# Performance work log

Measured on AMD Instinct MI355X. Metric: run time of the kernel, lower is better.

## Reference

```python
import jax, jax.numpy as jnp
import numpy as np

NUM_USERS = 100000
NUM_RATINGS = 5
EMBED_DIM = 64
ATT_DIM = 16
B, G, L, S = 16384, 8, 50, 32


def setup_inputs() -> dict:
    key = jax.random.key(0)
    ks = jax.random.split(key, 16)
    inp = {
        # forward args (int / bool constants)
        "nodes": jax.random.randint(ks[0], (B, G), 0, NUM_USERS),
        "history_u": jax.random.randint(ks[1], (B, L), 0, NUM_USERS),
        "history_r": jax.random.randint(ks[2], (B, L), 0, NUM_RATINGS),
        "history_mask": jax.random.randint(ks[3], (B, L), 0, 2).astype(bool).at[:, 0].set(True),
        "social_adj": jax.random.randint(ks[4], (B, S), 0, NUM_USERS),
        "social_mask": jax.random.randint(ks[5], (B, S), 0, 2).astype(bool).at[:, 0].set(True),
        # learned parameters
        "features": jax.random.normal(ks[6], (NUM_USERS, EMBED_DIM), jnp.float32) * 0.02,
        "r_embed": jax.random.normal(ks[7], (NUM_RATINGS, EMBED_DIM), jnp.float32) * 0.02,
        "wg1": jax.random.normal(ks[8], (EMBED_DIM, ATT_DIM), jnp.float32) / np.sqrt(EMBED_DIM),
        "bg1": jnp.zeros((ATT_DIM,), jnp.float32),
        "wg2": jax.random.normal(ks[9], (ATT_DIM, 1), jnp.float32) / np.sqrt(ATT_DIM),
        "bg2": jnp.zeros((1,), jnp.float32),
        "w1": jax.random.normal(ks[10], (2 * EMBED_DIM, EMBED_DIM), jnp.float32) / np.sqrt(2 * EMBED_DIM),
        "b1": jnp.zeros((EMBED_DIM,), jnp.float32),
    }
    return inp


def _masked_mean(x, mask):
    # x: [B, N, D], mask: [B, N] float -> [B, D]
    denom = jnp.maximum(mask.sum(axis=1, keepdims=True), 1.0)
    return (x * mask[..., None]).sum(axis=1) / denom


def reference(nodes, history_u, history_r, history_mask, social_adj, social_mask,
              features, r_embed, wg1, bg1, wg2, bg2, w1, b1):
    dt = features.dtype
    # --- Group_Embedding: attention pooling over member embeddings ---
    members = features[nodes]                              # [B, G, D] gather
    h = jnp.tanh(members @ wg1 + bg1)                      # [B, G, 16]
    logits = (h @ wg2 + bg2)[..., 0]                       # [B, G]
    alpha = jax.nn.softmax(logits, axis=-1)
    self_feats = jnp.einsum('bg,bgd->bd', alpha, members)  # [B, D]

    # --- aggregator: ragged history (item+rating) + social neighbor means ---
    hm = history_mask.astype(dt)
    hist = features[history_u] + r_embed[history_r]        # [B, L, D] gather
    hist_mean = _masked_mean(hist, hm)                     # [B, D]

    sm = social_mask.astype(dt)
    soc_mean = _masked_mean(features[social_adj], sm)      # [B, D]

    neigh_feats = 0.5 * (hist_mean + soc_mean)             # [B, D]

    # --- concat -> linear -> relu ---
    combined = jnp.concatenate([self_feats, neigh_feats], axis=1)  # [B, 2D]
    return jax.nn.relu(combined @ w1 + b1)                 # [B, D]
```

## Files before the change

kernel.cpp:

```cpp
#include <hip/hip_runtime.h>
#include <cstdint>
#include <cstddef>

#define NUSERS 100000
#define BB 16384

static __device__ __forceinline__ float readlane_f(float v, int l) {
    return __uint_as_float(__builtin_amdgcn_readlane(__float_as_uint(v), l));
}
static __device__ __forceinline__ int readlane_i(int v, int l) {
    return __builtin_amdgcn_readlane(v, l);
}

__global__ __launch_bounds__(256) void k0_scores(
    const float* __restrict__ features, const float* __restrict__ wg1,
    const float* __restrict__ bg1, const float* __restrict__ wg2,
    const float* __restrict__ bg2, float* __restrict__ Q)
{
    __shared__ float frow[16 * 68];
    __shared__ float wg1t[16 * 68];
    const int tid = threadIdx.x;
    const int blk = blockIdx.x;
    const float* fbase = features + (size_t)blk * 16 * 64;
    for (int i = tid; i < 1024; i += 256) {
        frow[(i >> 6) * 68 + (i & 63)] = fbase[i];
        wg1t[(i & 15) * 68 + (i >> 4)] = wg1[i];
    }
    __syncthreads();
    const int k = tid & 15, ul = tid >> 4;
    float x = bg1[k];
    #pragma unroll
    for (int d4 = 0; d4 < 16; ++d4) {
        const float4 f = *(const float4*)&frow[ul * 68 + d4 * 4];
        const float4 w = *(const float4*)&wg1t[k * 68 + d4 * 4];
        x += f.x * w.x + f.y * w.y + f.z * w.z + f.w * w.w;
    }
    float xx = fminf(fmaxf(x, -9.f), 9.f);
    float e2 = __expf(2.f * xx);
    float th = (e2 - 1.f) / (e2 + 1.f);
    float t = th * wg2[k];
    t += __shfl_xor(t, 1);
    t += __shfl_xor(t, 2);
    t += __shfl_xor(t, 4);
    t += __shfl_xor(t, 8);
    if (k == 0) Q[blk * 16 + ul] = t + bg2[0];
}

__global__ __launch_bounds__(256) void k1_fuse(
    const int* __restrict__ nodes, const int* __restrict__ hist_u,
    const int* __restrict__ hist_r, const int* __restrict__ hist_m,
    const int* __restrict__ soc_a, const int* __restrict__ soc_m,
    const float* __restrict__ features, const float* __restrict__ r_embed,
    const float* __restrict__ Q, float* __restrict__ comb)
{
    __shared__ int hcomp[4][64];
    __shared__ int scomp[4][32];

    const int tid = threadIdx.x;
    const int lane = tid & 63;
    const int wv = tid >> 6;
    const int e = blockIdx.x * 4 + wv;

    const float re0 = r_embed[0 * 64 + lane];
    const float re1 = r_embed[1 * 64 + lane];
    const float re2 = r_embed[2 * 64 + lane];
    const float re3 = r_embed[3 * 64 + lane];
    const float re4 = r_embed[4 * 64 + lane];

    int nd = (lane < 8) ? nodes[e * 8 + lane] : 0;
    int hu = 0, hr = 0, hmv = 0;
    if (lane < 50) {
        hu  = hist_u[e * 50 + lane];
        hr  = hist_r[e * 50 + lane];
        hmv = hist_m[e * 50 + lane];
    }
    int sa = 0, sk = 0;
    if (lane < 32) {
        sa = soc_a[e * 32 + lane];
        sk = soc_m[e * 32 + lane];
    }

    uint64_t hb = __ballot(hmv != 0);
    const int hc = (int)__popcll(hb);
    int hrank = (int)__popcll(hb & ((1ull << lane) - 1));
    if (hmv) hcomp[wv][hrank] = hu << 8;

    uint64_t sbm = __ballot(sk != 0);
    const int scn = (int)__popcll(sbm);
    int srank = (int)__popcll(sbm & ((1ull << lane) - 1));
    if (sk) scomp[wv][srank] = sa << 8;

    const int c0 = (int)__popcll(__ballot(hmv && hr == 0));
    const int c1 = (int)__popcll(__ballot(hmv && hr == 1));
    const int c2 = (int)__popcll(__ballot(hmv && hr == 2));
    const int c3 = (int)__popcll(__ballot(hmv && hr == 3));
    const int c4 = (int)__popcll(__ballot(hmv && hr == 4));

    float m[8];
    #pragma unroll
    for (int g = 0; g < 8; ++g) {
        int idx = readlane_i(nd, g);
        m[g] = features[idx * 64 + lane];
    }
    float sc = (lane < 8) ? Q[nd] : -1e30f;
    float mx = sc;
    mx = fmaxf(mx, __shfl_xor(mx, 1));
    mx = fmaxf(mx, __shfl_xor(mx, 2));
    mx = fmaxf(mx, __shfl_xor(mx, 4));
    float ex = __expf(sc - mx);
    float sm = ex;
    sm += __shfl_xor(sm, 1);
    sm += __shfl_xor(sm, 2);
    sm += __shfl_xor(sm, 4);
    float al = ex / sm;
    float sf = 0.f;
    #pragma unroll
    for (int g = 0; g < 8; ++g)
        sf += readlane_f(al, g) * m[g];

    int hpk = hcomp[wv][lane];
    int spk = scomp[wv][lane & 31];

    float a0 = 0.f, a1 = 0.f, a2 = 0.f, a3 = 0.f;
    int i = 0;
    for (; i + 4 <= hc; i += 4) {
        const float* r0 = (const float*)((const char*)features + (unsigned)readlane_i(hpk, i));
        const float* r1 = (const float*)((const char*)features + (unsigned)readlane_i(hpk, i + 1));
        const float* r2 = (const float*)((const char*)features + (unsigned)readlane_i(hpk, i + 2));
        const float* r3 = (const float*)((const char*)features + (unsigned)readlane_i(hpk, i + 3));
        a0 += r0[lane];
        a1 += r1[lane];
        a2 += r2[lane];
        a3 += r3[lane];
    }
    for (; i < hc; ++i) {
        const float* r0 = (const float*)((const char*)features + (unsigned)readlane_i(hpk, i));
        a0 += r0[lane];
    }
    float hsum = (a0 + a1) + (a2 + a3);
    hsum += (float)c0 * re0;
    hsum += (float)c1 * re1;
    hsum += (float)c2 * re2;
    hsum += (float)c3 * re3;
    hsum += (float)c4 * re4;
    float hmean = hsum / (float)hc;

    float s0 = 0.f, s1 = 0.f, s2 = 0.f, s3 = 0.f;
    i = 0;
    for (; i + 4 <= scn; i += 4) {
        const float* r0 = (const float*)((const char*)features + (unsigned)readlane_i(spk, i));
        const float* r1 = (const float*)((const char*)features + (unsigned)readlane_i(spk, i + 1));
        const float* r2 = (const float*)((const char*)features + (unsigned)readlane_i(spk, i + 2));
        const float* r3 = (const float*)((const char*)features + (unsigned)readlane_i(spk, i + 3));
        s0 += r0[lane];
        s1 += r1[lane];
        s2 += r2[lane];
        s3 += r3[lane];
    }
    for (; i < scn; ++i) {
        const float* r0 = (const float*)((const char*)features + (unsigned)readlane_i(spk, i));
        s0 += r0[lane];
    }
    float smean = ((s0 + s1) + (s2 + s3)) / (float)scn;

    comb[(size_t)e * 128 + lane] = sf;
    comb[(size_t)e * 128 + 64 + lane] = 0.5f * (hmean + smean);
}

__global__ __launch_bounds__(256) void k2_gemm(
    const float* __restrict__ comb, const float* __restrict__ w1,
    const float* __restrict__ b1, float* __restrict__ out)
{
    __shared__ float w1s[128 * 64];
    __shared__ float4 ct4[32 * 32];
    const int tid = threadIdx.x;
    const float4* w14 = (const float4*)w1;
    float4* w1s4 = (float4*)w1s;
    for (int i = tid; i < 2048; i += 256) w1s4[i] = w14[i];
    const float4* c4 = (const float4*)(comb + (size_t)blockIdx.x * 32 * 128);
    for (int i = tid; i < 1024; i += 256) ct4[i] = c4[i];
    __syncthreads();

    const int n = tid & 63, wv = tid >> 6;
    const float bv = b1[n];
    float acc[8] = {bv, bv, bv, bv, bv, bv, bv, bv};
    #pragma unroll
    for (int k4 = 0; k4 < 32; ++k4) {
        float w0  = w1s[(k4 * 4 + 0) * 64 + n];
        float w1v = w1s[(k4 * 4 + 1) * 64 + n];
        float w2v = w1s[(k4 * 4 + 2) * 64 + n];
        float w3v = w1s[(k4 * 4 + 3) * 64 + n];
        #pragma unroll
        for (int i = 0; i < 8; ++i) {
            float4 cv = ct4[(wv * 8 + i) * 32 + k4];
            acc[i] += cv.x * w0 + cv.y * w1v + cv.z * w2v + cv.w * w3v;
        }
    }
    const int row0 = blockIdx.x * 32 + wv * 8;
    #pragma unroll
    for (int i = 0; i < 8; ++i)
        out[(size_t)(row0 + i) * 64 + n] = fmaxf(acc[i], 0.f);
}

extern "C" void kernel_launch(void* const* d_in, const int* in_sizes, int n_in,
                              void* d_out, int out_size, void* d_ws, size_t ws_size,
                              hipStream_t stream)
{
    const int*   nodes    = (const int*)d_in[0];
    const int*   hu       = (const int*)d_in[1];
    const int*   hr       = (const int*)d_in[2];
    const int*   hm       = (const int*)d_in[3];
    const int*   sa       = (const int*)d_in[4];
    const int*   smk      = (const int*)d_in[5];
    const float* features = (const float*)d_in[6];
    const float* r_embed  = (const float*)d_in[7];
    const float* wg1      = (const float*)d_in[8];
    const float* bg1      = (const float*)d_in[9];
    const float* wg2      = (const float*)d_in[10];
    const float* bg2      = (const float*)d_in[11];
    const float* w1       = (const float*)d_in[12];
    const float* b1       = (const float*)d_in[13];
    float* out = (float*)d_out;

    float* Q    = (float*)d_ws;
    float* comb = Q + 131072;

    k0_scores<<<NUSERS / 16, 256, 0, stream>>>(features, wg1, bg1, wg2, bg2, Q);
    k1_fuse<<<BB / 4, 256, 0, stream>>>(nodes, hu, hr, hm, sa, smk,
                                        features, r_embed, Q, comb);
    k2_gemm<<<BB / 32, 256, 0, stream>>>(comb, w1, b1, out);
}
```

Measured before the change: 149.6 us.

## Gather embedding rows with float4 loads, four rows per wave instruction

Restructures the gather loops in the fused kernel so each 16-lane group loads one 64-float row with float4 vector loads. A single wave load instruction therefore fetches four different rows, and the partial sums from the four groups are combined with cross-lane shuffles at the end. This is meant to cut the number of scalar gather instructions and expose more memory-level parallelism. In exchange it adds shuffle reductions, predicated tail handling, and zero-initialisation of the shared index buffers so masked tail lanes read a valid row.

```diff
diff --git a/kernel.cpp b/kernel.cpp
--- a/kernel.cpp
+++ b/kernel.cpp
@@ -60,12 +60,19 @@
     const int lane = tid & 63;
     const int wv = tid >> 6;
     const int e = blockIdx.x * 4 + wv;
-
-    const float re0 = r_embed[0 * 64 + lane];
-    const float re1 = r_embed[1 * 64 + lane];
-    const float re2 = r_embed[2 * 64 + lane];
-    const float re3 = r_embed[3 * 64 + lane];
-    const float re4 = r_embed[4 * 64 + lane];
+    const int sub = lane & 15;
+    const int grp = lane >> 4;
+    const char* fbase = (const char*)features;
+
+    hcomp[wv][lane] = 0;
+    scomp[wv][lane & 31] = 0;
+
+    const float4* re4p = (const float4*)r_embed;
+    const float4 re0 = re4p[0 * 16 + sub];
+    const float4 re1 = re4p[1 * 16 + sub];
+    const float4 re2 = re4p[2 * 16 + sub];
+    const float4 re3 = re4p[3 * 16 + sub];
+    const float4 re4 = re4p[4 * 16 + sub];
 
     int nd = (lane < 8) ? nodes[e * 8 + lane] : 0;
     int hu = 0, hr = 0, hmv = 0;
@@ -96,12 +103,6 @@
     const int c3 = (int)__popcll(__ballot(hmv && hr == 3));
     const int c4 = (int)__popcll(__ballot(hmv && hr == 4));
 
-    float m[8];
-    #pragma unroll
-    for (int g = 0; g < 8; ++g) {
-        int idx = readlane_i(nd, g);
-        m[g] = features[idx * 64 + lane];
-    }
     float sc = (lane < 8) ? Q[nd] : -1e30f;
     float mx = sc;
     mx = fmaxf(mx, __shfl_xor(mx, 1));
@@ -113,58 +114,80 @@
     sm += __shfl_xor(sm, 2);
     sm += __shfl_xor(sm, 4);
     float al = ex / sm;
-    float sf = 0.f;
-    #pragma unroll
-    for (int g = 0; g < 8; ++g)
-        sf += readlane_f(al, g) * m[g];
 
     int hpk = hcomp[wv][lane];
     int spk = scomp[wv][lane & 31];
 
-    float a0 = 0.f, a1 = 0.f, a2 = 0.f, a3 = 0.f;
-    int i = 0;
-    for (; i + 4 <= hc; i += 4) {
-        const float* r0 = (const float*)((const char*)features + (unsigned)readlane_i(hpk, i));
-        const float* r1 = (const float*)((const char*)features + (unsigned)readlane_i(hpk, i + 1));
-        const float* r2 = (const float*)((const char*)features + (unsigned)readlane_i(hpk, i + 2));
-        const float* r3 = (const float*)((const char*)features + (unsigned)readlane_i(hpk, i + 3));
-        a0 += r0[lane];
-        a1 += r1[lane];
-        a2 += r2[lane];
-        a3 += r3[lane];
-    }
-    for (; i < hc; ++i) {
-        const float* r0 = (const float*)((const char*)features + (unsigned)readlane_i(hpk, i));
-        a0 += r0[lane];
-    }
-    float hsum = (a0 + a1) + (a2 + a3);
-    hsum += (float)c0 * re0;
-    hsum += (float)c1 * re1;
-    hsum += (float)c2 * re2;
-    hsum += (float)c3 * re3;
-    hsum += (float)c4 * re4;
-    float hmean = hsum / (float)hc;
-
-    float s0 = 0.f, s1 = 0.f, s2 = 0.f, s3 = 0.f;
-    i = 0;
-    for (; i + 4 <= scn; i += 4) {
-        const float* r0 = (const float*)((const char*)features + (unsigned)readlane_i(spk, i));
-        const float* r1 = (const float*)((const char*)features + (unsigned)readlane_i(spk, i + 1));
-        const float* r2 = (const float*)((const char*)features + (unsigned)readlane_i(spk, i + 2));
-        const float* r3 = (const float*)((const char*)features + (unsigned)readlane_i(spk, i + 3));
-        s0 += r0[lane];
-        s1 += r1[lane];
-        s2 += r2[lane];
-        s3 += r3[lane];
-    }
-    for (; i < scn; ++i) {
-        const float* r0 = (const float*)((const char*)features + (unsigned)readlane_i(spk, i));
-        s0 += r0[lane];
-    }
-    float smean = ((s0 + s1) + (s2 + s3)) / (float)scn;
-
-    comb[(size_t)e * 128 + lane] = sf;
-    comb[(size_t)e * 128 + 64 + lane] = 0.5f * (hmean + smean);
+    float4 sf4;
+    {
+        float a0 = __shfl(al, grp);
+        int   u0 = __shfl(nd, grp);
+        float a1 = __shfl(al, 4 + grp);
+        int   u1 = __shfl(nd, 4 + grp);
+        const float4 v0 = *(const float4*)(fbase + ((unsigned)u0 << 8) + sub * 16);
+        const float4 v1 = *(const float4*)(fbase + ((unsigned)u1 << 8) + sub * 16);
+        sf4.x = a0 * v0.x + a1 * v1.x;
+        sf4.y = a0 * v0.y + a1 * v1.y;
+        sf4.z = a0 * v0.z + a1 * v1.z;
+        sf4.w = a0 * v0.w + a1 * v1.w;
+    }
+
+    float4 ha4 = {0.f, 0.f, 0.f, 0.f};
+    const int hfull = hc & ~3;
+    for (int i = 0; i < hfull; i += 4) {
+        int off = __shfl(hpk, i + grp);
+        const float4 v = *(const float4*)(fbase + (unsigned)off + sub * 16);
+        ha4.x += v.x; ha4.y += v.y; ha4.z += v.z; ha4.w += v.w;
+    }
+    if (hfull < hc) {
+        int idx = hfull + grp;
+        int off = __shfl(hpk, idx);
+        float w = (idx < hc) ? 1.f : 0.f;
+        const float4 v = *(const float4*)(fbase + (unsigned)off + sub * 16);
+        ha4.x += w * v.x; ha4.y += w * v.y; ha4.z += w * v.z; ha4.w += w * v.w;
+    }
+
+    float4 sa4 = {0.f, 0.f, 0.f, 0.f};
+    const int sfull = scn & ~3;
+    for (int i = 0; i < sfull; i += 4) {
+        int off = __shfl(spk, i + grp);
+        const float4 v = *(const float4*)(fbase + (unsigned)off + sub * 16);
+        sa4.x += v.x; sa4.y += v.y; sa4.z += v.z; sa4.w += v.w;
+    }
+    if (sfull < scn) {
+        int idx = sfull + grp;
+        int off = __shfl(spk, idx);
+        float w = (idx < scn) ? 1.f : 0.f;
+        const float4 v = *(const float4*)(fbase + (unsigned)off + sub * 16);
+        sa4.x += w * v.x; sa4.y += w * v.y; sa4.z += w * v.z; sa4.w += w * v.w;
+    }
+
+#define XRED(v4)                                            \
+    v4.x += __shfl_xor(v4.x, 16); v4.x += __shfl_xor(v4.x, 32); \
+    v4.y += __shfl_xor(v4.y, 16); v4.y += __shfl_xor(v4.y, 32); \
+    v4.z += __shfl_xor(v4.z, 16); v4.z += __shfl_xor(v4.z, 32); \
+    v4.w += __shfl_xor(v4.w, 16); v4.w += __shfl_xor(v4.w, 32);
+    XRED(sf4)
+    XRED(ha4)
+    XRED(sa4)
+#undef XRED
+
+    float f0 = (float)c0, f1 = (float)c1, f2 = (float)c2, f3 = (float)c3, f4 = (float)c4;
+    ha4.x += f0 * re0.x + f1 * re1.x + f2 * re2.x + f3 * re3.x + f4 * re4.x;
+    ha4.y += f0 * re0.y + f1 * re1.y + f2 * re2.y + f3 * re3.y + f4 * re4.y;
+    ha4.z += f0 * re0.z + f1 * re1.z + f2 * re2.z + f3 * re3.z + f4 * re4.z;
+    ha4.w += f0 * re0.w + f1 * re1.w + f2 * re2.w + f3 * re3.w + f4 * re4.w;
+
+    const float ih = 1.f / (float)hc;
+    const float is = 1.f / (float)scn;
+    float4 nb4;
+    nb4.x = 0.5f * (ha4.x * ih + sa4.x * is);
+    nb4.y = 0.5f * (ha4.y * ih + sa4.y * is);
+    nb4.z = 0.5f * (ha4.z * ih + sa4.z * is);
+    nb4.w = 0.5f * (ha4.w * ih + sa4.w * is);
+
+    if (grp == 0) *(float4*)(comb + (size_t)e * 128 + sub * 4) = sf4;
+    if (grp == 1) *(float4*)(comb + (size_t)e * 128 + 64 + sub * 4) = nb4;
 }
 
 __global__ __launch_bounds__(256) void k2_gemm(
```

Result: no change. 149.8 us (+0.1%).
